# Kernel optimization log

Measured on AMD Instinct MI355X. Metric: run time of the kernel, lower is better.

## Reference

```python
import jax, jax.numpy as jnp
import numpy as np

N_NODES = 100000
N_EDGES = 1600000
F_IN = 128
HID = 128
N_CLS = 40


def _glorot(key, shape):
    fan_in, fan_out = shape[0], shape[1]
    lim = (6.0 / (fan_in + fan_out)) ** 0.5
    return jax.random.uniform(key, shape, jnp.float32, -lim, lim)


def setup_inputs() -> dict:
    key = jax.random.key(0)
    ks = jax.random.split(key, 10)
    x = jax.random.normal(ks[0], (N_NODES, F_IN), jnp.float32)
    edge_index = jax.random.randint(ks[1], (2, N_EDGES), 0, N_NODES, jnp.int64)
    return {
        "x": x,
        "edge_index": edge_index,
        "W1l": _glorot(ks[2], (F_IN, HID)),   # applied to aggregated neighbors
        "W1r": _glorot(ks[3], (F_IN, HID)),   # applied to root features
        "b1": jnp.zeros((HID,), jnp.float32),
        "W2l": _glorot(ks[4], (HID, HID)),
        "W2r": _glorot(ks[5], (HID, HID)),
        "b2": jnp.zeros((HID,), jnp.float32),
        "Wout": _glorot(ks[6], (HID, N_CLS)),
        "bout": jnp.zeros((N_CLS,), jnp.float32),
    }


def _sage_conv(x, src, dst, Wl, Wr, b):
    # mean aggregation of neighbor messages x[src] at dst, then linear combine
    msgs = x[src]                                                   # [E, F] gather
    agg = jax.ops.segment_sum(msgs, dst, num_segments=N_NODES)      # [N, F]
    cnt = jax.ops.segment_sum(jnp.ones((src.shape[0],), x.dtype), dst,
                              num_segments=N_NODES)                 # [N]
    agg = agg / jnp.maximum(cnt, 1.0)[:, None]
    return agg @ Wl + x @ Wr + b


def reference(x, edge_index, W1l, W1r, b1, W2l, W2r, b2, Wout, bout):
    src, dst = edge_index[0], edge_index[1]
    h = jax.nn.relu(_sage_conv(x, src, dst, W1l, W1r, b1))
    # dropout is identity in deterministic (eval) reference
    h = jax.nn.relu(_sage_conv(h, src, dst, W2l, W2r, b2))
    return h @ Wout + bout
```

## Files before the change

kernel.cpp:

```cpp
#include <hip/hip_runtime.h>
#include <hip/hip_bf16.h>

#define N_NODES 100000
#define N_EDGES 1600000
#define FDIM 128
#define NCLS 40
#define NCLS_PAD 48

#define NBINS ((N_NODES + 255) / 256)
#define NBLKB 256
#define CHUNKB (N_EDGES / NBLKB)
#define SCANTOT (NBINS * NBLKB)
#define SCANB_NB ((SCANTOT + 1023) / 1024)

#define LPAD 136

#define PACK1 (FDIM * 256)
#define PACK2 (FDIM * 256)
#define PACK3 (NCLS_PAD * FDIM)
#define PACKTOT (PACK1 + PACK2 + PACK3)
#define PACK_NB ((PACKTOT + 255) / 256)
#define CVT_N4 (N_NODES * FDIM / 4)
#define CVT_NB ((CVT_N4 + 255) / 256)

typedef __attribute__((ext_vector_type(8))) short short8;
typedef __attribute__((ext_vector_type(4))) float f32x4;

__device__ __forceinline__ float bf2f(unsigned short u) {
    union { unsigned int i; float f; } v; v.i = ((unsigned int)u) << 16; return v.f;
}
__device__ __forceinline__ unsigned short f2bf(float f) {
    __hip_bfloat16 h = __float2bfloat16(f);
    return *reinterpret_cast<unsigned short*>(&h);
}

__device__ __forceinline__ void pack_one(const float* Wl, const float* Wr, const float* bin,
                                         unsigned short* Bp, float* bout,
                                         int ncols_out, int ncols_src, int Keach, int idx) {
    int K = (Wr != nullptr) ? 2 * Keach : Keach;
    int col = idx / K, k = idx % K;
    float v = 0.f;
    if (col < ncols_src)
        v = (k < Keach) ? Wl[(size_t)k * ncols_src + col]
                        : Wr[(size_t)(k - Keach) * ncols_src + col];
    Bp[((size_t)(k >> 3) * ncols_out + col) * 8 + (k & 7)] = f2bf(v);
    if (k == 0) bout[col] = (col < ncols_src) ? bin[col] : 0.f;
}

__global__ __launch_bounds__(256) void k_prologue(
        const int* __restrict__ dst, int* __restrict__ bh,
        const float4* __restrict__ x4, ushort4* __restrict__ xb4,
        const float* __restrict__ W1l, const float* __restrict__ W1r,
        const float* __restrict__ b1, unsigned short* __restrict__ Bp1, float* __restrict__ b1p,
        const float* __restrict__ W2l, const float* __restrict__ W2r,
        const float* __restrict__ b2, unsigned short* __restrict__ Bp2, float* __restrict__ b2p,
        const float* __restrict__ Wout, const float* __restrict__ bo,
        unsigned short* __restrict__ Bp3, float* __restrict__ b3p) {
    __shared__ unsigned h[NBINS];
    int b = blockIdx.x;
    if (b < NBLKB) {
        for (int r = threadIdx.x; r < NBINS; r += 256) h[r] = 0u;
        __syncthreads();
        int base = b * CHUNKB;
        int end = base + CHUNKB; if (end > N_EDGES) end = N_EDGES;
        for (int e = base + threadIdx.x; e < end; e += 256)
            atomicAdd(&h[dst[e] >> 8], 1u);
        __syncthreads();
        for (int r = threadIdx.x; r < NBINS; r += 256)
            bh[b * NBINS + r] = (int)h[r];
        return;
    }
    b -= NBLKB;
    if (b < CVT_NB) {
        int i = b * 256 + threadIdx.x;
        if (i < CVT_N4) {
            float4 v = x4[i];
            ushort4 o;
            o.x = f2bf(v.x); o.y = f2bf(v.y); o.z = f2bf(v.z); o.w = f2bf(v.w);
            xb4[i] = o;
        }
        return;
    }
    b -= CVT_NB;
    int idx = b * 256 + threadIdx.x;
    if (idx < PACK1) { pack_one(W1l, W1r, b1, Bp1, b1p, FDIM, FDIM, FDIM, idx); return; }
    idx -= PACK1;
    if (idx < PACK2) { pack_one(W2l, W2r, b2, Bp2, b2p, FDIM, FDIM, FDIM, idx); return; }
    idx -= PACK2;
    if (idx < PACK3) { pack_one(Wout, nullptr, bo, Bp3, b3p, NCLS_PAD, NCLS, FDIM, idx); }
}

__global__ __launch_bounds__(1024) void k_scanB1(const int* __restrict__ bh,
                                                 int* __restrict__ obh,
                                                 unsigned* __restrict__ bsumB) {
    __shared__ unsigned wsums[16];
    int t = threadIdx.x;
    int wave = t >> 6, lane = t & 63;
    int g = blockIdx.x * 1024 + t;
    unsigned v = 0u;
    int r = g >> 8, b = g & (NBLKB - 1);
    if (g < SCANTOT) v = (unsigned)bh[b * NBINS + r];
    unsigned val = v;
#pragma unroll
    for (int d = 1; d < 64; d <<= 1) {
        unsigned n = __shfl_up(val, d, 64);
        if (lane >= d) val += n;
    }
    if (lane == 63) wsums[wave] = val;
    __syncthreads();
    if (t < 16) {
        unsigned wv = wsums[t];
#pragma unroll
        for (int d = 1; d < 16; d <<= 1) {
            unsigned n = __shfl_up(wv, d, 64);
            if (t >= d) wv += n;
        }
        wsums[t] = wv;
    }
    __syncthreads();
    unsigned waveoff = (wave > 0) ? wsums[wave - 1] : 0u;
    if (g < SCANTOT) obh[b * NBINS + r] = (int)(waveoff + val - v);
    if (t == 1023) bsumB[blockIdx.x] = wsums[15];
}

__global__ __launch_bounds__(1024) void k_scanB3(int* __restrict__ obh,
                                                 const unsigned* __restrict__ bsumB,
                                                 int* __restrict__ bucketbase) {
    __shared__ unsigned soff[SCANB_NB];
    int t = threadIdx.x;
    if (t < SCANB_NB) soff[t] = bsumB[t];
    __syncthreads();
    if (t == 0) {
        unsigned run = 0;
        for (int i = 0; i < SCANB_NB; ++i) { unsigned v = soff[i]; soff[i] = run; run += v; }
    }
    __syncthreads();
    int g = blockIdx.x * 1024 + t;
    if (g < SCANTOT) {
        int r = g >> 8, b = g & (NBLKB - 1);
        int val = obh[b * NBINS + r] + (int)soff[blockIdx.x];
        obh[b * NBINS + r] = val;
        if (b == 0) bucketbase[r] = val;
    }
    if (g == 0) bucketbase[NBINS] = N_EDGES;
}

__global__ __launch_bounds__(256) void k_binwriteB(const int* __restrict__ src, const int* __restrict__ dst,
                                                   const int* __restrict__ obh,
                                                   unsigned* __restrict__ bpack) {
    __shared__ unsigned pos[NBINS];
    for (int r = threadIdx.x; r < NBINS; r += 256)
        pos[r] = (unsigned)obh[blockIdx.x * NBINS + r];
    __syncthreads();
    int base = blockIdx.x * CHUNKB;
    int end = base + CHUNKB; if (end > N_EDGES) end = N_EDGES;
    for (int e = base + threadIdx.x; e < end; e += 256) {
        int d = dst[e];
        unsigned p = atomicAdd(&pos[d >> 8], 1u);
        bpack[p] = ((unsigned)(d & 255) << 24) | (unsigned)src[e];
    }
}

__global__ __launch_bounds__(256) void k_bucket_csr(const unsigned* __restrict__ bpack,
                                                    const int* __restrict__ bucketbase,
                                                    int* __restrict__ rowptr,
                                                    int* __restrict__ esrc) {
    __shared__ unsigned c[256];
    __shared__ unsigned ws[4];
    int b = blockIdx.x;
    int t = threadIdx.x;
    int wave = t >> 6, lane = t & 63;
    int bb = bucketbase[b], be = bucketbase[b + 1];
    c[t] = 0u;
    __syncthreads();
    for (int i = bb + t; i < be; i += 256)
        atomicAdd(&c[bpack[i] >> 24], 1u);
    __syncthreads();
    unsigned own = c[t];
    unsigned val = own;
#pragma unroll
    for (int d = 1; d < 64; d <<= 1) {
        unsigned n = __shfl_up(val, d, 64);
        if (lane >= d) val += n;
    }
    if (lane == 63) ws[wave] = val;
    __syncthreads();
    if (t < 4) {
        unsigned wv = ws[t];
#pragma unroll
        for (int d = 1; d < 4; d <<= 1) {
            unsigned n = __shfl_up(wv, d, 64);
            if (t >= d) wv += n;
        }
        ws[t] = wv;
    }
    __syncthreads();
    unsigned excl = ((wave > 0) ? ws[wave - 1] : 0u) + val - own;
    int node = (b << 8) + t;
    if (node < N_NODES) rowptr[node] = bb + (int)excl;
    if (b == NBINS - 1 && t == 0) rowptr[N_NODES] = N_EDGES;
    __syncthreads();
    c[t] = excl;
    __syncthreads();
    for (int i = bb + t; i < be; i += 256) {
        unsigned p = bpack[i];
        unsigned slot = atomicAdd(&c[p >> 24], 1u);
        esrc[bb + (int)slot] = (int)(p & 0x00FFFFFFu);
    }
}

__global__ __launch_bounds__(256, 8) void k_aggregate(
                            const unsigned short* __restrict__ feat,
                            const int* __restrict__ esrc,
                            const int* __restrict__ rowptr,
                            unsigned short* __restrict__ out) {
    int node = blockIdx.x * 4 + (threadIdx.x >> 6);
    if (node >= N_NODES) return;
    int lane = threadIdx.x & 63;
    int sub = lane >> 4;
    int fl = lane & 15;
    int s = rowptr[node], e = rowptr[node + 1];
    float a0[8], a1[8];
#pragma unroll
    for (int q = 0; q < 8; ++q) { a0[q] = 0.f; a1[q] = 0.f; }

    int j = s + sub;
    for (; j + 4 < e; j += 8) {
        int sv0 = esrc[j];
        int sv1 = esrc[j + 4];
        short8 v0 = *(const short8*)(feat + (size_t)sv0 * FDIM + fl * 8);
        short8 v1 = *(const short8*)(feat + (size_t)sv1 * FDIM + fl * 8);
#pragma unroll
        for (int q = 0; q < 8; ++q) {
            a0[q] += bf2f((unsigned short)v0[q]);
            a1[q] += bf2f((unsigned short)v1[q]);
        }
    }
    if (j < e) {
        int sv = esrc[j];
        short8 v = *(const short8*)(feat + (size_t)sv * FDIM + fl * 8);
#pragma unroll
        for (int q = 0; q < 8; ++q) a0[q] += bf2f((unsigned short)v[q]);
    }
#pragma unroll
    for (int q = 0; q < 8; ++q) a0[q] += a1[q];
#pragma unroll
    for (int q = 0; q < 8; ++q) {
        a0[q] += __shfl_xor(a0[q], 16, 64);
        a0[q] += __shfl_xor(a0[q], 32, 64);
    }
    int deg = e - s;
    float inv = 1.0f / (float)(deg > 1 ? deg : 1);
    if (sub == 0) {
        short8 o;
#pragma unroll
        for (int q = 0; q < 8; ++q) o[q] = (short)f2bf(a0[q] * inv);
        *(short8*)(out + (size_t)node * FDIM + fl * 8) = o;
    }
}

__global__ __launch_bounds__(256) void k_gemm_layer(
        const unsigned short* __restrict__ A0, const unsigned short* __restrict__ A1,
        const unsigned short* __restrict__ Bp, const float* __restrict__ bias,
        unsigned short* __restrict__ out) {
    int wave = threadIdx.x >> 6;
    int lane = threadIdx.x & 63;
    int rowblk = blockIdx.x * 64 + wave * 16;
    int lrow = lane & 15;
    int kgrp = lane >> 4;
    int arow = rowblk + lrow; if (arow > N_NODES - 1) arow = N_NODES - 1;

    f32x4 acc[8];
#pragma unroll
    for (int c = 0; c < 8; ++c) acc[c] = (f32x4){0.f, 0.f, 0.f, 0.f};

#pragma unroll
    for (int kb = 0; kb < 8; ++kb) {
        const unsigned short* Asrc = (kb < 4) ? A0 : A1;
        int kk = (kb & 3) * 32 + kgrp * 8;
        short8 a = *(const short8*)(Asrc + (size_t)arow * FDIM + kk);
        int k8 = kb * 4 + kgrp;
        const unsigned short* brow = Bp + ((size_t)k8 * FDIM + lrow) * 8;
#pragma unroll
        for (int c = 0; c < 8; ++c) {
            short8 b = *(const short8*)(brow + c * 16 * 8);
            acc[c] = __builtin_amdgcn_mfma_f32_16x16x32_bf16(a, b, acc[c], 0, 0, 0);
        }
    }

    int orowbase = rowblk + kgrp * 4;
#pragma unroll
    for (int c = 0; c < 8; ++c) {
        int col = c * 16 + lrow;
        float bv = bias[col];
#pragma unroll
        for (int i = 0; i < 4; ++i) {
            int r = orowbase + i;
            if (r < N_NODES) {
                float v = acc[c][i] + bv;
                v = fmaxf(v, 0.f);
                out[(size_t)r * FDIM + col] = f2bf(v);
            }
        }
    }
}

__global__ __launch_bounds__(256) void k_gemm_final(
        const unsigned short* __restrict__ A0, const unsigned short* __restrict__ A1,
        const unsigned short* __restrict__ Bp, const float* __restrict__ bias,
        const unsigned short* __restrict__ Bp3, const float* __restrict__ bias3,
        float* __restrict__ out) {
    __shared__ unsigned short Alds[4][16][LPAD];
    int wave = threadIdx.x >> 6;
    int lane = threadIdx.x & 63;
    int rowblk = blockIdx.x * 64 + wave * 16;
    int lrow = lane & 15;
    int kgrp = lane >> 4;
    int arow = rowblk + lrow; if (arow > N_NODES - 1) arow = N_NODES - 1;

    f32x4 acc2[8];
#pragma unroll
    for (int c = 0; c < 8; ++c) acc2[c] = (f32x4){0.f, 0.f, 0.f, 0.f};

#pragma unroll
    for (int kb = 0; kb < 8; ++kb) {
        const unsigned short* Asrc = (kb < 4) ? A0 : A1;
        int kk = (kb & 3) * 32 + kgrp * 8;
        short8 a = *(const short8*)(Asrc + (size_t)arow * FDIM + kk);
        int k8 = kb * 4 + kgrp;
        const unsigned short* brow = Bp + ((size_t)k8 * FDIM + lrow) * 8;
#pragma unroll
        for (int c = 0; c < 8; ++c) {
            short8 b = *(const short8*)(brow + c * 16 * 8);
            acc2[c] = __builtin_amdgcn_mfma_f32_16x16x32_bf16(a, b, acc2[c], 0, 0, 0);
        }
    }

    int srowbase = kgrp * 4;
#pragma unroll
    for (int c = 0; c < 8; ++c) {
        int col = c * 16 + lrow;
        float bv = bias[col];
#pragma unroll
        for (int i = 0; i < 4; ++i) {
            float v = acc2[c][i] + bv;
            v = fmaxf(v, 0.f);
            Alds[wave][srowbase + i][col] = f2bf(v);
        }
    }

    f32x4 acc3[3];
#pragma unroll
    for (int c = 0; c < 3; ++c) acc3[c] = (f32x4){0.f, 0.f, 0.f, 0.f};

#pragma unroll
    for (int kb = 0; kb < 4; ++kb) {
        short8 a = *(const short8*)(&Alds[wave][lrow][kb * 32 + kgrp * 8]);
        int k8 = kb * 4 + kgrp;
        const unsigned short* brow = Bp3 + ((size_t)k8 * NCLS_PAD + lrow) * 8;
#pragma unroll
        for (int c = 0; c < 3; ++c) {
            short8 b = *(const short8*)(brow + c * 16 * 8);
            acc3[c] = __builtin_amdgcn_mfma_f32_16x16x32_bf16(a, b, acc3[c], 0, 0, 0);
        }
    }

    int orowbase = rowblk + kgrp * 4;
#pragma unroll
    for (int c = 0; c < 3; ++c) {
        int col = c * 16 + lrow;
        if (col < NCLS) {
            float bv = bias3[col];
#pragma unroll
            for (int i = 0; i < 4; ++i) {
                int r = orowbase + i;
                if (r < N_NODES)
                    out[(size_t)r * NCLS + col] = acc3[c][i] + bv;
            }
        }
    }
}

extern "C" void kernel_launch(void* const* d_in, const int* in_sizes, int n_in,
                              void* d_out, int out_size, void* d_ws, size_t ws_size,
                              hipStream_t stream) {
    const float* x    = (const float*)d_in[0];
    const int*   ei   = (const int*)d_in[1];
    const float* W1l  = (const float*)d_in[2];
    const float* W1r  = (const float*)d_in[3];
    const float* b1   = (const float*)d_in[4];
    const float* W2l  = (const float*)d_in[5];
    const float* W2r  = (const float*)d_in[6];
    const float* b2   = (const float*)d_in[7];
    const float* Wout = (const float*)d_in[8];
    const float* bout = (const float*)d_in[9];
    const int* src = ei;
    const int* dst = ei + N_EDGES;

    char* ws = (char*)d_ws;
    size_t off = 0;
    auto alloc = [&](size_t bytes) -> void* {
        void* p = ws + off;
        off += (bytes + 255) & ~(size_t)255;
        return p;
    };
    unsigned short* xb   = (unsigned short*)alloc((size_t)N_NODES * FDIM * 2);
    unsigned short* aggn = (unsigned short*)alloc((size_t)N_NODES * FDIM * 2);
    unsigned short* h1   = (unsigned short*)alloc((size_t)N_NODES * FDIM * 2);
    unsigned short* Bp1  = (unsigned short*)alloc((size_t)FDIM * 256 * 2);
    unsigned short* Bp2  = (unsigned short*)alloc((size_t)FDIM * 256 * 2);
    unsigned short* Bp3  = (unsigned short*)alloc((size_t)NCLS_PAD * FDIM * 2);
    float* b1p = (float*)alloc(FDIM * 4);
    float* b2p = (float*)alloc(FDIM * 4);
    float* b3p = (float*)alloc(NCLS_PAD * 4);
    int* rowptr    = (int*)alloc((size_t)(N_NODES + 1) * 4);
    int* esrc      = (int*)alloc((size_t)N_EDGES * 4);
    int* bh        = (int*)alloc((size_t)NBLKB * NBINS * 4);
    int* obh       = (int*)alloc((size_t)NBLKB * NBINS * 4);
    int* bucketbase= (int*)alloc((size_t)(NBINS + 1) * 4);
    unsigned* bsumB = (unsigned*)alloc((size_t)SCANB_NB * 4);
    unsigned* bpack = (unsigned*)alloc((size_t)N_EDGES * 4);

    int proGrid = NBLKB + CVT_NB + PACK_NB;
    k_prologue<<<proGrid, 256, 0, stream>>>(
        dst, bh, (const float4*)x, (ushort4*)xb,
        W1l, W1r, b1, Bp1, b1p, W2l, W2r, b2, Bp2, b2p, Wout, bout, Bp3, b3p);

    k_scanB1<<<SCANB_NB, 1024, 0, stream>>>(bh, obh, bsumB);
    k_scanB3<<<SCANB_NB, 1024, 0, stream>>>(obh, bsumB, bucketbase);
    k_binwriteB<<<NBLKB, 256, 0, stream>>>(src, dst, obh, bpack);
    k_bucket_csr<<<NBINS, 256, 0, stream>>>(bpack, bucketbase, rowptr, esrc);

    int aggGrid = (N_NODES + 3) / 4;
    int gemmGrid = (N_NODES + 63) / 64;

    k_aggregate<<<aggGrid, 256, 0, stream>>>(xb, esrc, rowptr, aggn);
    k_gemm_layer<<<gemmGrid, 256, 0, stream>>>(aggn, xb, Bp1, b1p, h1);
    k_aggregate<<<aggGrid, 256, 0, stream>>>(h1, esrc, rowptr, aggn);
    k_gemm_final<<<gemmGrid, 256, 0, stream>>>(aggn, h1, Bp2, b2p, Bp3, b3p, (float*)d_out);
}
```

Baseline: 234.6 us.

## Fuse CSR scan, bin-write and bucket sort into one cooperative kernel

Replaces four separate CSR-building launches (two scan passes, bin write, bucket CSR) with one cooperative kernel of NBINS blocks that uses grid-wide syncs between phases. The scan is restructured so each block scans one bin's per-chunk counts, then every block redundantly scans the bin totals. This removes three kernel launch gaps and the bucketbase buffer, at the cost of grid.sync overhead and a requirement that all 391 blocks are co-resident.

```diff
diff --git a/kernel.cpp b/kernel.cpp
--- a/kernel.cpp
+++ b/kernel.cpp
@@ -1,5 +1,8 @@
 #include <hip/hip_runtime.h>
 #include <hip/hip_bf16.h>
+#include <hip/hip_cooperative_groups.h>
+
+namespace cg = cooperative_groups;
 
 #define N_NODES 100000
 #define N_EDGES 1600000
@@ -10,8 +13,6 @@
 #define NBINS ((N_NODES + 255) / 256)
 #define NBLKB 256
 #define CHUNKB (N_EDGES / NBLKB)
-#define SCANTOT (NBINS * NBLKB)
-#define SCANB_NB ((SCANTOT + 1023) / 1024)
 
 #define LPAD 136
 
@@ -90,122 +91,109 @@
     if (idx < PACK3) { pack_one(Wout, nullptr, bo, Bp3, b3p, NCLS_PAD, NCLS, FDIM, idx); }
 }
 
-__global__ __launch_bounds__(1024) void k_scanB1(const int* __restrict__ bh,
-                                                 int* __restrict__ obh,
-                                                 unsigned* __restrict__ bsumB) {
-    __shared__ unsigned wsums[16];
+__global__ __launch_bounds__(256) void k_csr_coop(
+        const int* __restrict__ src, const int* __restrict__ dst,
+        const int* __restrict__ bh, int* __restrict__ obh,
+        unsigned* __restrict__ bsz, unsigned* __restrict__ bpack,
+        int* __restrict__ rowptr, int* __restrict__ esrc) {
+    cg::grid_group grid = cg::this_grid();
+    int blk = blockIdx.x;
     int t = threadIdx.x;
     int wave = t >> 6, lane = t & 63;
-    int g = blockIdx.x * 1024 + t;
-    unsigned v = 0u;
-    int r = g >> 8, b = g & (NBLKB - 1);
-    if (g < SCANTOT) v = (unsigned)bh[b * NBINS + r];
-    unsigned val = v;
-#pragma unroll
-    for (int d = 1; d < 64; d <<= 1) {
-        unsigned n = __shfl_up(val, d, 64);
-        if (lane >= d) val += n;
-    }
-    if (lane == 63) wsums[wave] = val;
-    __syncthreads();
-    if (t < 16) {
-        unsigned wv = wsums[t];
-#pragma unroll
-        for (int d = 1; d < 16; d <<= 1) {
-            unsigned n = __shfl_up(wv, d, 64);
-            if (t >= d) wv += n;
-        }
-        wsums[t] = wv;
-    }
-    __syncthreads();
-    unsigned waveoff = (wave > 0) ? wsums[wave - 1] : 0u;
-    if (g < SCANTOT) obh[b * NBINS + r] = (int)(waveoff + val - v);
-    if (t == 1023) bsumB[blockIdx.x] = wsums[15];
-}
-
-__global__ __launch_bounds__(1024) void k_scanB3(int* __restrict__ obh,
-                                                 const unsigned* __restrict__ bsumB,
-                                                 int* __restrict__ bucketbase) {
-    __shared__ unsigned soff[SCANB_NB];
-    int t = threadIdx.x;
-    if (t < SCANB_NB) soff[t] = bsumB[t];
-    __syncthreads();
-    if (t == 0) {
-        unsigned run = 0;
-        for (int i = 0; i < SCANB_NB; ++i) { unsigned v = soff[i]; soff[i] = run; run += v; }
-    }
-    __syncthreads();
-    int g = blockIdx.x * 1024 + t;
-    if (g < SCANTOT) {
-        int r = g >> 8, b = g & (NBLKB - 1);
-        int val = obh[b * NBINS + r] + (int)soff[blockIdx.x];
-        obh[b * NBINS + r] = val;
-        if (b == 0) bucketbase[r] = val;
-    }
-    if (g == 0) bucketbase[NBINS] = N_EDGES;
-}
-
-__global__ __launch_bounds__(256) void k_binwriteB(const int* __restrict__ src, const int* __restrict__ dst,
-                                                   const int* __restrict__ obh,
-                                                   unsigned* __restrict__ bpack) {
+    __shared__ unsigned sh[512];
     __shared__ unsigned pos[NBINS];
-    for (int r = threadIdx.x; r < NBINS; r += 256)
-        pos[r] = (unsigned)obh[blockIdx.x * NBINS + r];
-    __syncthreads();
-    int base = blockIdx.x * CHUNKB;
-    int end = base + CHUNKB; if (end > N_EDGES) end = N_EDGES;
-    for (int e = base + threadIdx.x; e < end; e += 256) {
-        int d = dst[e];
-        unsigned p = atomicAdd(&pos[d >> 8], 1u);
-        bpack[p] = ((unsigned)(d & 255) << 24) | (unsigned)src[e];
-    }
-}
-
-__global__ __launch_bounds__(256) void k_bucket_csr(const unsigned* __restrict__ bpack,
-                                                    const int* __restrict__ bucketbase,
-                                                    int* __restrict__ rowptr,
-                                                    int* __restrict__ esrc) {
-    __shared__ unsigned c[256];
-    __shared__ unsigned ws[4];
-    int b = blockIdx.x;
-    int t = threadIdx.x;
-    int wave = t >> 6, lane = t & 63;
-    int bb = bucketbase[b], be = bucketbase[b + 1];
-    c[t] = 0u;
-    __syncthreads();
-    for (int i = bb + t; i < be; i += 256)
-        atomicAdd(&c[bpack[i] >> 24], 1u);
-    __syncthreads();
-    unsigned own = c[t];
-    unsigned val = own;
-#pragma unroll
-    for (int d = 1; d < 64; d <<= 1) {
-        unsigned n = __shfl_up(val, d, 64);
-        if (lane >= d) val += n;
-    }
-    if (lane == 63) ws[wave] = val;
-    __syncthreads();
-    if (t < 4) {
-        unsigned wv = ws[t];
-#pragma unroll
-        for (int d = 1; d < 4; d <<= 1) {
-            unsigned n = __shfl_up(wv, d, 64);
-            if (t >= d) wv += n;
-        }
-        ws[t] = wv;
-    }
-    __syncthreads();
-    unsigned excl = ((wave > 0) ? ws[wave - 1] : 0u) + val - own;
-    int node = (b << 8) + t;
-    if (node < N_NODES) rowptr[node] = bb + (int)excl;
-    if (b == NBINS - 1 && t == 0) rowptr[N_NODES] = N_EDGES;
-    __syncthreads();
-    c[t] = excl;
-    __syncthreads();
-    for (int i = bb + t; i < be; i += 256) {
-        unsigned p = bpack[i];
-        unsigned slot = atomicAdd(&c[p >> 24], 1u);
-        esrc[bb + (int)slot] = (int)(p & 0x00FFFFFFu);
+    __shared__ unsigned ws4[4];
+
+    {
+        unsigned v = (unsigned)bh[t * NBINS + blk];
+        unsigned val = v;
+#pragma unroll
+        for (int d = 1; d < 64; d <<= 1) { unsigned n = __shfl_up(val, d, 64); if (lane >= d) val += n; }
+        if (lane == 63) ws4[wave] = val;
+        __syncthreads();
+        if (t < 4) {
+            unsigned wv = ws4[t];
+#pragma unroll
+            for (int d = 1; d < 4; d <<= 1) { unsigned n = __shfl_up(wv, d, 64); if (t >= d) wv += n; }
+            ws4[t] = wv;
+        }
+        __syncthreads();
+        unsigned incl = ((wave > 0) ? ws4[wave - 1] : 0u) + val;
+        obh[t * NBINS + blk] = (int)(incl - v);
+        if (t == 255) bsz[blk] = incl;
+    }
+    grid.sync();
+
+    {
+        int i0 = 2 * t, i1 = 2 * t + 1;
+        unsigned a = (i0 < NBINS) ? bsz[i0] : 0u;
+        unsigned b2 = (i1 < NBINS) ? bsz[i1] : 0u;
+        unsigned s2 = a + b2;
+        unsigned val = s2;
+#pragma unroll
+        for (int d = 1; d < 64; d <<= 1) { unsigned n = __shfl_up(val, d, 64); if (lane >= d) val += n; }
+        if (lane == 63) ws4[wave] = val;
+        __syncthreads();
+        if (t < 4) {
+            unsigned wv = ws4[t];
+#pragma unroll
+            for (int d = 1; d < 4; d <<= 1) { unsigned n = __shfl_up(wv, d, 64); if (t >= d) wv += n; }
+            ws4[t] = wv;
+        }
+        __syncthreads();
+        unsigned excl2 = ((wave > 0) ? ws4[wave - 1] : 0u) + val - s2;
+        if (i0 < NBINS) sh[i0] = excl2;
+        if (i1 < NBINS) sh[i1] = excl2 + a;
+        __syncthreads();
+    }
+
+    if (blk < NBLKB) {
+        for (int r = t; r < NBINS; r += 256)
+            pos[r] = sh[r] + (unsigned)obh[blk * NBINS + r];
+        __syncthreads();
+        int base = blk * CHUNKB;
+        int end = base + CHUNKB; if (end > N_EDGES) end = N_EDGES;
+        for (int e = base + t; e < end; e += 256) {
+            int d = dst[e];
+            unsigned p = atomicAdd(&pos[d >> 8], 1u);
+            bpack[p] = ((unsigned)(d & 255) << 24) | (unsigned)src[e];
+        }
+    }
+    grid.sync();
+
+    {
+        int bb = (int)sh[blk];
+        int be = (blk + 1 < NBINS) ? (int)sh[blk + 1] : N_EDGES;
+        pos[t] = 0u;
+        __syncthreads();
+        for (int i = bb + t; i < be; i += 256)
+            atomicAdd(&pos[bpack[i] >> 24], 1u);
+        __syncthreads();
+        unsigned own = pos[t];
+        unsigned val = own;
+#pragma unroll
+        for (int d = 1; d < 64; d <<= 1) { unsigned n = __shfl_up(val, d, 64); if (lane >= d) val += n; }
+        if (lane == 63) ws4[wave] = val;
+        __syncthreads();
+        if (t < 4) {
+            unsigned wv = ws4[t];
+#pragma unroll
+            for (int d = 1; d < 4; d <<= 1) { unsigned n = __shfl_up(wv, d, 64); if (t >= d) wv += n; }
+            ws4[t] = wv;
+        }
+        __syncthreads();
+        unsigned excl = ((wave > 0) ? ws4[wave - 1] : 0u) + val - own;
+        int node = (blk << 8) + t;
+        if (node < N_NODES) rowptr[node] = bb + (int)excl;
+        if (blk == NBINS - 1 && t == 0) rowptr[N_NODES] = N_EDGES;
+        __syncthreads();
+        pos[t] = excl;
+        __syncthreads();
+        for (int i = bb + t; i < be; i += 256) {
+            unsigned p = bpack[i];
+            unsigned slot = atomicAdd(&pos[p >> 24], 1u);
+            esrc[bb + (int)slot] = (int)(p & 0x00FFFFFFu);
+        }
     }
 }
 
@@ -417,8 +405,7 @@
     int* esrc      = (int*)alloc((size_t)N_EDGES * 4);
     int* bh        = (int*)alloc((size_t)NBLKB * NBINS * 4);
     int* obh       = (int*)alloc((size_t)NBLKB * NBINS * 4);
-    int* bucketbase= (int*)alloc((size_t)(NBINS + 1) * 4);
-    unsigned* bsumB = (unsigned*)alloc((size_t)SCANB_NB * 4);
+    unsigned* bsz  = (unsigned*)alloc((size_t)NBINS * 4);
     unsigned* bpack = (unsigned*)alloc((size_t)N_EDGES * 4);
 
     int proGrid = NBLKB + CVT_NB + PACK_NB;
@@ -426,10 +413,12 @@
         dst, bh, (const float4*)x, (ushort4*)xb,
         W1l, W1r, b1, Bp1, b1p, W2l, W2r, b2, Bp2, b2p, Wout, bout, Bp3, b3p);
 
-    k_scanB1<<<SCANB_NB, 1024, 0, stream>>>(bh, obh, bsumB);
-    k_scanB3<<<SCANB_NB, 1024, 0, stream>>>(obh, bsumB, bucketbase);
-    k_binwriteB<<<NBLKB, 256, 0, stream>>>(src, dst, obh, bpack);
-    k_bucket_csr<<<NBINS, 256, 0, stream>>>(bpack, bucketbase, rowptr, esrc);
+    {
+        void* args[] = { (void*)&src, (void*)&dst, (void*)&bh, (void*)&obh,
+                         (void*)&bsz, (void*)&bpack, (void*)&rowptr, (void*)&esrc };
+        hipLaunchCooperativeKernel((void*)k_csr_coop, dim3(NBINS), dim3(256),
+                                   args, 0, stream);
+    }
 
     int aggGrid = (N_NODES + 3) / 4;
     int gemmGrid = (N_NODES + 63) / 64;
```

Result: slower. 333.3 us (+42.1%).
